# Optimization experiments

Measured on AMD Instinct MI355X. Metric: run time of the kernel, lower is better.

## Reference

```python
import jax, jax.numpy as jnp
import numpy as np
import math

B, T, C, H = 2, 2048, 1024, 16
D = C // H  # head dim = 64
ROPE_BASE = 10000.0


def _rope(x):
    # x: (B, T, H, D); interleaved-pair RoPE matching torch apply_rope
    theta = jnp.exp(jnp.arange(0, D, 2, dtype=jnp.float32) * (-math.log(ROPE_BASE) / D))  # (D/2,)
    ang = jnp.arange(T, dtype=jnp.float32)[:, None] * theta[None, :]  # (T, D/2)
    cos = jnp.cos(ang)[None, :, None, :]  # (1, T, 1, D/2)
    sin = jnp.sin(ang)[None, :, None, :]
    xr = x.reshape(B, T, H, D // 2, 2)
    x0, x1 = xr[..., 0], xr[..., 1]
    out = jnp.stack([x0 * cos - x1 * sin, x1 * cos + x0 * sin], axis=-1)
    return out.reshape(B, T, H, D).astype(x.dtype)


def setup_inputs() -> dict:
    key = jax.random.key(0)
    k0, k1, k2 = jax.random.split(key, 3)
    x = jax.random.normal(k0, (B, T, C), dtype=jnp.float32)
    Wqkv = jax.random.normal(k1, (3 * C, C), dtype=jnp.float32) * 0.02
    bqkv = jnp.zeros((3 * C,), dtype=jnp.float32)
    Wproj = jax.random.normal(k2, (C, C), dtype=jnp.float32) * 0.02
    bproj = jnp.zeros((C,), dtype=jnp.float32)
    return {"x": x, "Wqkv": Wqkv, "bqkv": bqkv, "Wproj": Wproj, "bproj": bproj}


def reference(x, Wqkv, bqkv, Wproj, bproj):
    qkv = x @ Wqkv.T + bqkv  # (B, T, 3C)
    q, k, v = jnp.split(qkv, 3, axis=-1)
    q = _rope(q.reshape(B, T, H, D)).transpose(0, 2, 1, 3)  # (B, H, T, D)
    k = _rope(k.reshape(B, T, H, D)).transpose(0, 2, 1, 3)
    v = v.reshape(B, T, H, D).transpose(0, 2, 1, 3)
    scores = jnp.einsum('bhqd,bhkd->bhqk', q, k) * (1.0 / math.sqrt(D))
    causal = jnp.tril(jnp.ones((T, T), dtype=bool))  # (T, T)
    scores = jnp.where(causal[None, None, :, :], scores, -jnp.inf)
    attn = jax.nn.softmax(scores, axis=-1)
    y = jnp.einsum('bhqk,bhkd->bhqd', attn, v)  # (B, H, T, D)
    y = y.transpose(0, 2, 1, 3).reshape(B, T, C)
    return y @ Wproj.T + bproj
```

## Files before the change

kernel.cpp:

```cpp
#include <hip/hip_runtime.h>

typedef unsigned short u16;
typedef unsigned int u32;
typedef __bf16 bf16x8 __attribute__((ext_vector_type(8)));
typedef float f32x4 __attribute__((ext_vector_type(4)));
typedef float f32x16 __attribute__((ext_vector_type(16)));

#define BB 2
#define TT 2048
#define CC 1024
#define HH 16
#define DD 64
#define MR (BB*TT)
#define NQ (3*CC)
#define SCQ 0.18033688f

__device__ __forceinline__ u16 f2b(float f) {
    u32 u = __builtin_bit_cast(u32, f);
    u = (u + 0x7fffu + ((u >> 16) & 1u)) >> 16;
    return (u16)u;
}
__device__ __forceinline__ float b2f(u16 b) {
    return __builtin_bit_cast(float, (u32)b << 16);
}
__device__ __forceinline__ u32 pkbf(float a, float b) {
    ushort2 t; t.x = f2b(a); t.y = f2b(b);
    return __builtin_bit_cast(u32, t);
}

__device__ __forceinline__ void gll16(const void* g, void* l) {
    __builtin_amdgcn_global_load_lds(
        (const __attribute__((address_space(1))) void*)g,
        (__attribute__((address_space(3))) void*)l,
        16, 0, 0);
}

__global__ void cvt_all(const float* __restrict__ x, const float* __restrict__ wqkv,
                        const float* __restrict__ wproj,
                        u16* __restrict__ xb, u16* __restrict__ wqkvb, u16* __restrict__ wprojb,
                        float2* __restrict__ tab, u32* __restrict__ ctr)
{
    if (blockIdx.x == 0 && threadIdx.x == 0) *ctr = 0;
    const int n0 = MR * CC / 4, n1 = NQ * CC / 4, n2 = CC * CC / 4;
    int i = blockIdx.x * 256 + threadIdx.x;
    if (i < n0 + n1 + n2) {
        const float* src; u16* dst; int off;
        if (i < n0)           { src = x;     dst = xb;     off = i; }
        else if (i < n0 + n1) { src = wqkv;  dst = wqkvb;  off = i - n0; }
        else                  { src = wproj; dst = wprojb; off = i - n0 - n1; }
        float4 v = reinterpret_cast<const float4*>(src)[off];
        ushort4 o;
        o.x = f2b(v.x); o.y = f2b(v.y); o.z = f2b(v.z); o.w = f2b(v.w);
        reinterpret_cast<ushort4*>(dst)[off] = o;
    } else {
        const int e = i - (n0 + n1 + n2);
        if (e < TT * 32) {
            const int t = e >> 5, j = e & 31;
            const float theta = expf((float)(2 * j) * (-0.14391157f));
            float s, c;
            sincosf((float)t * theta, &s, &c);
            tab[e] = make_float2(c, s);
        }
    }
}

__global__ __launch_bounds__(256) void gemm_qkv(
    const u16* __restrict__ A, const u16* __restrict__ Bm,
    const float* __restrict__ bias, const float2* __restrict__ tab,
    u16* __restrict__ Qr, u16* __restrict__ Kr, u16* __restrict__ Vc)
{
    __shared__ __align__(16) u16 As[128 * 32];
    __shared__ __align__(16) u16 Bs[128 * 32];
    const int K = CC;
    const int tid = threadIdx.x;
    const int lane = tid & 63;
    const int w = tid >> 6;
    const int wr = w >> 1, wc = w & 1;
    const int fr = lane & 15, fq = lane >> 4;
    const int orig = blockIdx.y * 24 + blockIdx.x;
    const int wg = (orig & 7) * 96 + (orig >> 3);
    const int brow = (wg / 24) * 128, bcol = (wg % 24) * 128;
    const int srow = lane >> 2;
    const int scol = (lane & 3) * 8;

    f32x4 acc[4][4];
    const f32x4 zero = {0.f, 0.f, 0.f, 0.f};
#pragma unroll
    for (int i = 0; i < 4; i++)
#pragma unroll
        for (int j = 0; j < 4; j++) acc[i][j] = zero;

    for (int kt = 0; kt < K; kt += 32) {
#pragma unroll
        for (int i = 0; i < 2; i++) {
            const int r = i * 64 + w * 16 + srow;
            gll16(&A[(size_t)(brow + r) * K + kt + scol], &As[(i * 64 + w * 16) * 32]);
            gll16(&Bm[(size_t)(bcol + r) * K + kt + scol], &Bs[(i * 64 + w * 16) * 32]);
        }
        __syncthreads();
        bf16x8 af[4], bfr[4];
#pragma unroll
        for (int mi = 0; mi < 4; mi++)
            af[mi] = *reinterpret_cast<const bf16x8*>(&As[(wr * 64 + mi * 16 + fr) * 32 + fq * 8]);
#pragma unroll
        for (int nj = 0; nj < 4; nj++)
            bfr[nj] = *reinterpret_cast<const bf16x8*>(&Bs[(wc * 64 + nj * 16 + fr) * 32 + fq * 8]);
#pragma unroll
        for (int mi = 0; mi < 4; mi++)
#pragma unroll
            for (int nj = 0; nj < 4; nj++)
                acc[mi][nj] = __builtin_amdgcn_mfma_f32_16x16x32_bf16(af[mi], bfr[nj], acc[mi][nj], 0, 0, 0);
        __syncthreads();
    }

#pragma unroll
    for (int mi = 0; mi < 4; mi++) {
#pragma unroll
        for (int nj = 0; nj < 4; nj++) {
            const int n = bcol + wc * 64 + nj * 16 + fr;
            const float bn = bias[n];
            const int sec = n >> 10;
            const int h = (n >> 6) & 15;
            const int d = n & 63;
            const int j = d >> 1;
            const bool odd = d & 1;
#pragma unroll
            for (int r = 0; r < 4; r++) {
                const int m = brow + wr * 64 + mi * 16 + fq * 4 + r;
                const int b = m >> 11, t = m & 2047;
                const float v = acc[mi][nj][r] + bn;
                const float p = __shfl_xor(v, 1);
                if (sec == 2) {
                    Vc[(size_t)m * CC + (n - 2 * CC)] = f2b(v);
                } else {
                    const float2 cs = tab[t * 32 + j];
                    const float o = odd ? (v * cs.x + p * cs.y) : (v * cs.x - p * cs.y);
                    const size_t oidx = ((size_t)(b * HH + h) * TT + t) * DD + d;
                    if (sec == 0) Qr[oidx] = f2b(o * SCQ);
                    else          Kr[oidx] = f2b(o);
                }
            }
        }
    }
}

template<int BF16_OUT>
__global__ __launch_bounds__(256) void gemm_bt(
    const u16* __restrict__ A, const u16* __restrict__ Bm,
    const float* __restrict__ bias, void* __restrict__ outp,
    int M, int N, int K)
{
    __shared__ __align__(16) u16 As[128 * 32];
    __shared__ __align__(16) u16 Bs[128 * 32];
    const int tid = threadIdx.x;
    const int lane = tid & 63;
    const int w = tid >> 6;
    const int wr = w >> 1, wc = w & 1;
    const int fr = lane & 15, fq = lane >> 4;
    const int brow = blockIdx.y * 128, bcol = blockIdx.x * 128;
    const int srow = lane >> 2;
    const int scol = (lane & 3) * 8;

    f32x4 acc[4][4];
    const f32x4 zero = {0.f, 0.f, 0.f, 0.f};
#pragma unroll
    for (int i = 0; i < 4; i++)
#pragma unroll
        for (int j = 0; j < 4; j++) acc[i][j] = zero;

    for (int kt = 0; kt < K; kt += 32) {
#pragma unroll
        for (int i = 0; i < 2; i++) {
            const int r = i * 64 + w * 16 + srow;
            gll16(&A[(size_t)(brow + r) * K + kt + scol], &As[(i * 64 + w * 16) * 32]);
            gll16(&Bm[(size_t)(bcol + r) * K + kt + scol], &Bs[(i * 64 + w * 16) * 32]);
        }
        __syncthreads();
        bf16x8 af[4], bfr[4];
#pragma unroll
        for (int mi = 0; mi < 4; mi++)
            af[mi] = *reinterpret_cast<const bf16x8*>(&As[(wr * 64 + mi * 16 + fr) * 32 + fq * 8]);
#pragma unroll
        for (int nj = 0; nj < 4; nj++)
            bfr[nj] = *reinterpret_cast<const bf16x8*>(&Bs[(wc * 64 + nj * 16 + fr) * 32 + fq * 8]);
#pragma unroll
        for (int mi = 0; mi < 4; mi++)
#pragma unroll
            for (int nj = 0; nj < 4; nj++)
                acc[mi][nj] = __builtin_amdgcn_mfma_f32_16x16x32_bf16(af[mi], bfr[nj], acc[mi][nj], 0, 0, 0);
        __syncthreads();
    }

#pragma unroll
    for (int mi = 0; mi < 4; mi++) {
#pragma unroll
        for (int nj = 0; nj < 4; nj++) {
            const int n = bcol + wc * 64 + nj * 16 + fr;
            const float bn = bias[n];
#pragma unroll
            for (int r = 0; r < 4; r++) {
                const int m = brow + wr * 64 + mi * 16 + fq * 4 + r;
                const float v = acc[mi][nj][r] + bn;
                if (BF16_OUT) reinterpret_cast<u16*>(outp)[(size_t)m * N + n] = f2b(v);
                else          reinterpret_cast<float*>(outp)[(size_t)m * N + n] = v;
            }
        }
    }
}

__global__ __launch_bounds__(64) void vtrans(const u16* __restrict__ Vc, u16* __restrict__ Vtg)
{
    const int lane = threadIdx.x;
    const int t0 = blockIdx.x * 64;
    const int bh = blockIdx.y;
    const int b = bh >> 4, h = bh & 15;
    u32 packed[32];
#pragma unroll
    for (int tt = 0; tt < 64; tt += 2) {
        const u16 a = Vc[(size_t)(b * TT + t0 + tt) * CC + h * DD + lane];
        const u16 c = Vc[(size_t)(b * TT + t0 + tt + 1) * CC + h * DD + lane];
        packed[tt >> 1] = (u32)a | ((u32)c << 16);
    }
    u32* dst = reinterpret_cast<u32*>(&Vtg[((size_t)bh * DD + lane) * TT + t0]);
#pragma unroll
    for (int i = 0; i < 32; i += 4)
        *reinterpret_cast<uint4*>(&dst[i]) = make_uint4(packed[i], packed[i + 1], packed[i + 2], packed[i + 3]);
}

__global__ __launch_bounds__(512) void attn_fwd(
    const u16* __restrict__ Q, const u16* __restrict__ Kg, const u16* __restrict__ Vtg,
    u16* __restrict__ Y, u32* __restrict__ ctr)
{
    __shared__ __align__(16) u16 smem[4 * 64 * 72];
    __shared__ int cur;
    const int tid = threadIdx.x;
    const int lane = tid & 63;
    const int ql = lane & 31;
    const int hB = lane >> 5;
    const int wq = (tid >> 6) & 3;
    const int g  = tid >> 8;
    const int srow = (tid & 255) >> 2;
    const int sc   = tid & 3;
    u16* KsG = smem + (g * 2 + 0) * 4608;
    u16* VsG = smem + (g * 2 + 1) * 4608;
    float* fm = reinterpret_cast<float*>(smem);

    while (true) {
        if (tid == 0) cur = atomicAdd(ctr, 1);
        __syncthreads();
        const int it = cur;
        __syncthreads();
        if (it >= 512) break;

        const int bx = 15 - (it >> 5);
        const int bh = it & 31;
        const int q0 = bx << 7;
        const int halfL = bx + 1;
        const int b = bh >> 4, hh = bh & 15;
        const int qb = q0 + wq * 32;
        const int qg = qb + ql;
        const size_t base  = (size_t)bh * TT * DD;
        const size_t vbase = (size_t)bh * DD * TT;

        bf16x8 qf[4];
#pragma unroll
        for (int ds = 0; ds < 4; ds++)
            qf[ds] = *reinterpret_cast<const bf16x8*>(&Q[base + (size_t)qg * DD + ds * 16 + hB * 8]);

        f32x16 acc[2];
#pragma unroll
        for (int dh = 0; dh < 2; dh++)
#pragma unroll
            for (int r = 0; r < 16; r++) acc[dh][r] = 0.f;
        float m_ = -1e30f, l_ = 0.f;

        int kv0 = 64 * g;
        uint4 kr0, kr1, vr0, vr1;
        {
            const size_t kro = base + (size_t)(kv0 + srow) * DD;
            kr0 = *reinterpret_cast<const uint4*>(&Kg[kro + sc * 8]);
            kr1 = *reinterpret_cast<const uint4*>(&Kg[kro + 32 + sc * 8]);
            const size_t vro = vbase + (size_t)srow * TT + kv0;
            vr0 = *reinterpret_cast<const uint4*>(&Vtg[vro + sc * 8]);
            vr1 = *reinterpret_cast<const uint4*>(&Vtg[vro + 32 + sc * 8]);
        }

        for (int i = 0; i < halfL; ++i) {
            *reinterpret_cast<uint4*>(&KsG[srow * 72 + sc * 8])      = kr0;
            *reinterpret_cast<uint4*>(&KsG[srow * 72 + 32 + sc * 8]) = kr1;
            *reinterpret_cast<uint4*>(&VsG[srow * 72 + sc * 8])      = vr0;
            *reinterpret_cast<uint4*>(&VsG[srow * 72 + 32 + sc * 8]) = vr1;
            if (i + 1 < halfL) {
                const size_t kro = base + (size_t)(kv0 + 128 + srow) * DD;
                kr0 = *reinterpret_cast<const uint4*>(&Kg[kro + sc * 8]);
                kr1 = *reinterpret_cast<const uint4*>(&Kg[kro + 32 + sc * 8]);
                const size_t vro = vbase + (size_t)srow * TT + kv0 + 128;
                vr0 = *reinterpret_cast<const uint4*>(&Vtg[vro + sc * 8]);
                vr1 = *reinterpret_cast<const uint4*>(&Vtg[vro + 32 + sc * 8]);
            }
            __syncthreads();

            if (kv0 <= qb + 31) {
                f32x16 sa[2];
#pragma unroll
                for (int st = 0; st < 2; st++)
#pragma unroll
                    for (int r = 0; r < 16; r++) sa[st][r] = 0.f;
                __builtin_amdgcn_s_setprio(1);
#pragma unroll
                for (int st = 0; st < 2; st++)
#pragma unroll
                    for (int ds = 0; ds < 4; ds++) {
                        bf16x8 kf = *reinterpret_cast<const bf16x8*>(
                            &KsG[(st * 32 + ql) * 72 + ds * 16 + hB * 8]);
                        sa[st] = __builtin_amdgcn_mfma_f32_32x32x16_bf16(kf, qf[ds], sa[st], 0, 0, 0);
                    }
                __builtin_amdgcn_s_setprio(0);
                if (kv0 + 63 > qb) {
#pragma unroll
                    for (int st = 0; st < 2; st++) {
                        const int kb0 = kv0 + st * 32 + 4 * hB;
#pragma unroll
                        for (int r = 0; r < 16; r++) {
                            const int kg = kb0 + (r & 3) + 8 * (r >> 2);
                            if (kg > qg) sa[st][r] = -1e30f;
                        }
                    }
                }
                float mx[16];
#pragma unroll
                for (int j = 0; j < 16; j++) mx[j] = fmaxf(sa[0][j], sa[1][j]);
#pragma unroll
                for (int j = 0; j < 8; j++) mx[j] = fmaxf(mx[j], mx[j + 8]);
#pragma unroll
                for (int j = 0; j < 4; j++) mx[j] = fmaxf(mx[j], mx[j + 4]);
                float tm = fmaxf(fmaxf(mx[0], mx[1]), fmaxf(mx[2], mx[3]));
                tm = fmaxf(tm, __shfl_xor(tm, 32));
                const float mn = fmaxf(m_, tm);
                const bool need = __any(mn > m_);
                float scl = 1.0f;
                if (need) { scl = exp2f(m_ - mn); m_ = mn; }
#pragma unroll
                for (int st = 0; st < 2; st++)
#pragma unroll
                    for (int r = 0; r < 16; r++)
                        sa[st][r] = exp2f(sa[st][r] - m_);
                float ps[16];
#pragma unroll
                for (int j = 0; j < 16; j++) ps[j] = sa[0][j] + sa[1][j];
#pragma unroll
                for (int j = 0; j < 8; j++) ps[j] += ps[j + 8];
#pragma unroll
                for (int j = 0; j < 4; j++) ps[j] += ps[j + 4];
                float rs = (ps[0] + ps[1]) + (ps[2] + ps[3]);
                rs += __shfl_xor(rs, 32);
                if (need) {
                    l_ = l_ * scl + rs;
#pragma unroll
                    for (int dh = 0; dh < 2; dh++)
#pragma unroll
                        for (int r = 0; r < 16; r++) acc[dh][r] *= scl;
                } else {
                    l_ += rs;
                }
                u32 pk[2][8];
#pragma unroll
                for (int st = 0; st < 2; st++)
#pragma unroll
                    for (int wd = 0; wd < 8; wd++)
                        pk[st][wd] = pkbf(sa[st][2 * wd], sa[st][2 * wd + 1]);
                __builtin_amdgcn_s_setprio(1);
#pragma unroll
                for (int c = 0; c < 4; c++) {
                    u32 a0 = pk[c >> 1][4 * (c & 1) + 0];
                    u32 a1 = pk[c >> 1][4 * (c & 1) + 1];
                    u32 a2 = pk[c >> 1][4 * (c & 1) + 2];
                    u32 a3 = pk[c >> 1][4 * (c & 1) + 3];
                    asm volatile("v_permlane32_swap_b32 %0, %1" : "+v"(a0), "+v"(a2));
                    asm volatile("v_permlane32_swap_b32 %0, %1" : "+v"(a1), "+v"(a3));
                    uint4 tw = make_uint4(a0, a1, a2, a3);
                    bf16x8 pb = __builtin_bit_cast(bf16x8, tw);
#pragma unroll
                    for (int dh = 0; dh < 2; dh++) {
                        bf16x8 vf = *reinterpret_cast<const bf16x8*>(
                            &VsG[(dh * 32 + ql) * 72 + c * 16 + hB * 8]);
                        acc[dh] = __builtin_amdgcn_mfma_f32_32x32x16_bf16(vf, pb, acc[dh], 0, 0, 0);
                    }
                }
                __builtin_amdgcn_s_setprio(0);
            }
            __syncthreads();
            kv0 += 128;
        }

        const int fidx = (wq * 64 + lane) * 36;
        if (g == 1) {
#pragma unroll
            for (int dh = 0; dh < 2; dh++)
#pragma unroll
                for (int r = 0; r < 16; r++) fm[fidx + dh * 16 + r] = acc[dh][r];
            fm[fidx + 32] = m_;
            fm[fidx + 33] = l_;
        }
        __syncthreads();
        float o_sc1 = 0.f, o_sc2 = 0.f, linv = 0.f;
        float acc2[32];
        if (g == 0) {
            const float m2 = fm[fidx + 32];
            const float l2 = fm[fidx + 33];
            const float mm = fmaxf(m_, m2);
            o_sc1 = exp2f(m_ - mm);
            o_sc2 = exp2f(m2 - mm);
            const float lt = l_ * o_sc1 + l2 * o_sc2;
            linv = 1.0f / lt;
#pragma unroll
            for (int dh = 0; dh < 2; dh++)
#pragma unroll
                for (int r = 0; r < 16; r++) acc2[dh * 16 + r] = fm[fidx + dh * 16 + r];
        }
        __syncthreads();
        if (g == 0) {
            const int lrow = wq * 32 + ql;
#pragma unroll
            for (int dh = 0; dh < 2; dh++)
#pragma unroll
                for (int rp = 0; rp < 16; rp += 2) {
                    const int d = (rp & 3) + 8 * (rp >> 2) + 4 * hB + 32 * dh;
                    const float v0 = (acc[dh][rp]     * o_sc1 + acc2[dh * 16 + rp]     * o_sc2) * linv;
                    const float v1 = (acc[dh][rp + 1] * o_sc1 + acc2[dh * 16 + rp + 1] * o_sc2) * linv;
                    *reinterpret_cast<u32*>(&smem[lrow * 72 + d]) = pkbf(v0, v1);
                }
        }
        __syncthreads();
        {
            const int row = tid >> 2;
            const int ch = tid & 3;
#pragma unroll
            for (int p = 0; p < 2; ++p) {
                uint4 ov = *reinterpret_cast<const uint4*>(&smem[row * 72 + (ch + 4 * p) * 8]);
                *reinterpret_cast<uint4*>(&Y[(size_t)(b * TT + q0 + row) * CC + hh * DD + (ch + 4 * p) * 8]) = ov;
            }
        }
        __syncthreads();
    }
}

extern "C" void kernel_launch(void* const* d_in, const int* in_sizes, int n_in,
                              void* d_out, int out_size, void* d_ws, size_t ws_size,
                              hipStream_t stream)
{
    const float* x     = (const float*)d_in[0];
    const float* Wqkv  = (const float*)d_in[1];
    const float* bqkv  = (const float*)d_in[2];
    const float* Wproj = (const float*)d_in[3];
    const float* bproj = (const float*)d_in[4];
    float* out = (float*)d_out;

    u16* ws     = (u16*)d_ws;
    u16* xb     = ws;
    u16* wqkvb  = xb     + (size_t)MR * CC;
    u16* wprojb = wqkvb  + (size_t)NQ * CC;
    u16* Vc     = wprojb + (size_t)CC * CC;
    u16* Qr     = Vc     + (size_t)MR * CC;
    u16* Kr     = Qr     + (size_t)BB * HH * TT * DD;
    u16* Vtg    = Kr     + (size_t)BB * HH * TT * DD;
    u16* yb     = Vtg    + (size_t)BB * HH * TT * DD;
    float2* tab = (float2*)(yb + (size_t)MR * CC);
    u32* ctr    = (u32*)(tab + (size_t)TT * 32);

    cvt_all<<<dim3(8448), 256, 0, stream>>>(x, Wqkv, Wproj, xb, wqkvb, wprojb, tab, ctr);

    gemm_qkv<<<dim3(24, 32), 256, 0, stream>>>(xb, wqkvb, bqkv, tab, Qr, Kr, Vc);

    vtrans<<<dim3(TT / 64, BB * HH), 64, 0, stream>>>(Vc, Vtg);

    attn_fwd<<<dim3(256), 512, 0, stream>>>(Qr, Kr, Vtg, yb, ctr);

    gemm_bt<0><<<dim3(CC / 128, MR / 128), 256, 0, stream>>>(yb, wprojb, bproj, out, MR, CC, CC);
}
```

Measured before the change: 212.7 us.

## Shrink projection GEMM tile, remap blocks, use native bf16 conversion and 3-input max

```diff
diff --git a/kernel.cpp b/kernel.cpp
--- a/kernel.cpp
+++ b/kernel.cpp
@@ -2,6 +2,7 @@
 
 typedef unsigned short u16;
 typedef unsigned int u32;
+typedef __bf16 bf16x2 __attribute__((ext_vector_type(2)));
 typedef __bf16 bf16x8 __attribute__((ext_vector_type(8)));
 typedef float f32x4 __attribute__((ext_vector_type(4)));
 typedef float f32x16 __attribute__((ext_vector_type(16)));
@@ -16,15 +17,14 @@
 #define SCQ 0.18033688f
 
 __device__ __forceinline__ u16 f2b(float f) {
-    u32 u = __builtin_bit_cast(u32, f);
-    u = (u + 0x7fffu + ((u >> 16) & 1u)) >> 16;
-    return (u16)u;
+    __bf16 h = (__bf16)f;
+    return __builtin_bit_cast(u16, h);
 }
 __device__ __forceinline__ float b2f(u16 b) {
     return __builtin_bit_cast(float, (u32)b << 16);
 }
 __device__ __forceinline__ u32 pkbf(float a, float b) {
-    ushort2 t; t.x = f2b(a); t.y = f2b(b);
+    bf16x2 t; t[0] = (__bf16)a; t[1] = (__bf16)b;
     return __builtin_bit_cast(u32, t);
 }
 
@@ -144,49 +144,48 @@
     }
 }
 
-template<int BF16_OUT>
-__global__ __launch_bounds__(256) void gemm_bt(
+__global__ __launch_bounds__(256) void gemm_proj(
     const u16* __restrict__ A, const u16* __restrict__ Bm,
-    const float* __restrict__ bias, void* __restrict__ outp,
-    int M, int N, int K)
-{
-    __shared__ __align__(16) u16 As[128 * 32];
+    const float* __restrict__ bias, float* __restrict__ outp)
+{
+    __shared__ __align__(16) u16 As[64 * 32];
     __shared__ __align__(16) u16 Bs[128 * 32];
+    const int M = MR, N = CC, K = CC;
     const int tid = threadIdx.x;
     const int lane = tid & 63;
     const int w = tid >> 6;
-    const int wr = w >> 1, wc = w & 1;
     const int fr = lane & 15, fq = lane >> 4;
-    const int brow = blockIdx.y * 128, bcol = blockIdx.x * 128;
+    const int orig = blockIdx.y * 8 + blockIdx.x;
+    const int wg = (orig & 7) * 64 + (orig >> 3);
+    const int brow = (wg >> 3) * 64, bcol = (wg & 7) * 128;
     const int srow = lane >> 2;
     const int scol = (lane & 3) * 8;
 
-    f32x4 acc[4][4];
+    f32x4 acc[4][2];
     const f32x4 zero = {0.f, 0.f, 0.f, 0.f};
 #pragma unroll
     for (int i = 0; i < 4; i++)
 #pragma unroll
-        for (int j = 0; j < 4; j++) acc[i][j] = zero;
+        for (int j = 0; j < 2; j++) acc[i][j] = zero;
 
     for (int kt = 0; kt < K; kt += 32) {
-#pragma unroll
-        for (int i = 0; i < 2; i++) {
-            const int r = i * 64 + w * 16 + srow;
-            gll16(&A[(size_t)(brow + r) * K + kt + scol], &As[(i * 64 + w * 16) * 32]);
-            gll16(&Bm[(size_t)(bcol + r) * K + kt + scol], &Bs[(i * 64 + w * 16) * 32]);
-        }
-        __syncthreads();
-        bf16x8 af[4], bfr[4];
+        gll16(&A[(size_t)(brow + w * 16 + srow) * K + kt + scol], &As[(w * 16) * 32]);
+#pragma unroll
+        for (int i = 0; i < 2; i++)
+            gll16(&Bm[(size_t)(bcol + i * 64 + w * 16 + srow) * K + kt + scol],
+                  &Bs[(i * 64 + w * 16) * 32]);
+        __syncthreads();
+        bf16x8 af[4], bfr[2];
 #pragma unroll
         for (int mi = 0; mi < 4; mi++)
-            af[mi] = *reinterpret_cast<const bf16x8*>(&As[(wr * 64 + mi * 16 + fr) * 32 + fq * 8]);
-#pragma unroll
-        for (int nj = 0; nj < 4; nj++)
-            bfr[nj] = *reinterpret_cast<const bf16x8*>(&Bs[(wc * 64 + nj * 16 + fr) * 32 + fq * 8]);
+            af[mi] = *reinterpret_cast<const bf16x8*>(&As[(mi * 16 + fr) * 32 + fq * 8]);
+#pragma unroll
+        for (int nj = 0; nj < 2; nj++)
+            bfr[nj] = *reinterpret_cast<const bf16x8*>(&Bs[(w * 32 + nj * 16 + fr) * 32 + fq * 8]);
 #pragma unroll
         for (int mi = 0; mi < 4; mi++)
 #pragma unroll
-            for (int nj = 0; nj < 4; nj++)
+            for (int nj = 0; nj < 2; nj++)
                 acc[mi][nj] = __builtin_amdgcn_mfma_f32_16x16x32_bf16(af[mi], bfr[nj], acc[mi][nj], 0, 0, 0);
         __syncthreads();
     }
@@ -194,15 +193,13 @@
 #pragma unroll
     for (int mi = 0; mi < 4; mi++) {
 #pragma unroll
-        for (int nj = 0; nj < 4; nj++) {
-            const int n = bcol + wc * 64 + nj * 16 + fr;
+        for (int nj = 0; nj < 2; nj++) {
+            const int n = bcol + w * 32 + nj * 16 + fr;
             const float bn = bias[n];
 #pragma unroll
             for (int r = 0; r < 4; r++) {
-                const int m = brow + wr * 64 + mi * 16 + fq * 4 + r;
-                const float v = acc[mi][nj][r] + bn;
-                if (BF16_OUT) reinterpret_cast<u16*>(outp)[(size_t)m * N + n] = f2b(v);
-                else          reinterpret_cast<float*>(outp)[(size_t)m * N + n] = v;
+                const int m = brow + mi * 16 + fq * 4 + r;
+                outp[(size_t)m * N + n] = acc[mi][nj][r] + bn;
             }
         }
     }
@@ -330,11 +327,14 @@
                 float mx[16];
 #pragma unroll
                 for (int j = 0; j < 16; j++) mx[j] = fmaxf(sa[0][j], sa[1][j]);
-#pragma unroll
-                for (int j = 0; j < 8; j++) mx[j] = fmaxf(mx[j], mx[j + 8]);
-#pragma unroll
-                for (int j = 0; j < 4; j++) mx[j] = fmaxf(mx[j], mx[j + 4]);
-                float tm = fmaxf(fmaxf(mx[0], mx[1]), fmaxf(mx[2], mx[3]));
+                const float r0 = fmaxf(fmaxf(mx[0], mx[1]), mx[2]);
+                const float r1 = fmaxf(fmaxf(mx[3], mx[4]), mx[5]);
+                const float r2 = fmaxf(fmaxf(mx[6], mx[7]), mx[8]);
+                const float r3 = fmaxf(fmaxf(mx[9], mx[10]), mx[11]);
+                const float r4 = fmaxf(fmaxf(mx[12], mx[13]), mx[14]);
+                const float r5 = fmaxf(fmaxf(r0, r1), r2);
+                const float r6 = fmaxf(fmaxf(r3, r4), mx[15]);
+                float tm = fmaxf(r5, r6);
                 tm = fmaxf(tm, __shfl_xor(tm, 32));
                 const float mn = fmaxf(m_, tm);
                 const bool need = __any(mn > m_);
@@ -476,5 +476,5 @@
 
     attn_fwd<<<dim3(256), 512, 0, stream>>>(Qr, Kr, Vtg, yb, ctr);
 
-    gemm_bt<0><<<dim3(CC / 128, MR / 128), 256, 0, stream>>>(yb, wprojb, bproj, out, MR, CC, CC);
-}
+    gemm_proj<<<dim3(8, 64), 256, 0, stream>>>(yb, wprojb, bproj, out);
+}
```

Result: faster. 202.3 us (-4.9%).
